# Kernel tuning notes

Measured on AMD Instinct MI355X. Metric: run time of the kernel, lower is better.

## Reference

```python
import jax, jax.numpy as jnp
import numpy as np

N, D, E, EDGE_DIM = 50000, 128, 800000, 3
NEG_SLOPE = 0.2
LN_EPS = 1e-5


def setup_inputs() -> dict:
    key = jax.random.key(0)
    ks = jax.random.split(key, 12)
    s = 1.0 / np.sqrt(D)
    return {
        "x": jax.random.normal(ks[0], (N, D), jnp.float32),
        "edge_index": jax.random.randint(ks[1], (2, E), 0, N, jnp.int32),
        "edge_attr": jax.random.normal(ks[2], (E, EDGE_DIM), jnp.float32),
        "W_l": jax.random.normal(ks[3], (D, D), jnp.float32) * s,
        "b_l": jnp.zeros((D,), jnp.float32),
        "W_r": jax.random.normal(ks[4], (D, D), jnp.float32) * s,
        "b_r": jnp.zeros((D,), jnp.float32),
        "W_e": jax.random.normal(ks[5], (EDGE_DIM, D), jnp.float32) * (1.0 / np.sqrt(EDGE_DIM)),
        "att": jax.random.normal(ks[6], (D,), jnp.float32) * s,
        "bias": jnp.zeros((D,), jnp.float32),
        "res_weight": jnp.array(0.1, jnp.float32),
        "ln_gamma": jnp.ones((D,), jnp.float32),
        "ln_beta": jnp.zeros((D,), jnp.float32),
    }


def reference(x, edge_index, edge_attr, W_l, b_l, W_r, b_r, W_e, att, bias,
              res_weight, ln_gamma, ln_beta):
    src, dst = edge_index[0], edge_index[1]
    # GATv2: lin_l on source, lin_r on target (heads=1, concat=False)
    x_l = x @ W_l + b_l            # [N, D]
    x_r = x @ W_r + b_r            # [N, D]
    e_emb = edge_attr @ W_e        # [E, D]
    # per-edge attention logits
    m = x_l[src] + x_r[dst] + e_emb                      # [E, D]
    m = jnp.where(m > 0, m, NEG_SLOPE * m)               # leaky_relu(0.2)
    alpha = m @ att                                       # [E]
    # segment softmax over destination nodes
    seg_max = jax.ops.segment_max(alpha, dst, num_segments=N)
    seg_max = jnp.where(jnp.isfinite(seg_max), seg_max, 0.0)
    ex = jnp.exp(alpha - seg_max[dst])
    seg_sum = jax.ops.segment_sum(ex, dst, num_segments=N)
    alpha = ex / (seg_sum[dst] + 1e-16)                   # [E]
    # weighted aggregation of transformed source features (dropout off / eval)
    msgs = x_l[src] * alpha[:, None]                      # [E, D]
    out = jax.ops.segment_sum(msgs, dst, num_segments=N) + bias  # [N, D]
    # residual + LayerNorm
    out = x + res_weight * out
    mu = jnp.mean(out, axis=-1, keepdims=True)
    var = jnp.mean(jnp.square(out - mu), axis=-1, keepdims=True)
    out = (out - mu) * jax.lax.rsqrt(var + LN_EPS)
    return out * ln_gamma + ln_beta
```

## Files before the change

kernel.cpp:

```cpp
#include <hip/hip_runtime.h>
#include <hip/hip_bf16.h>

#define N_NODES 50000
#define DIM 128
#define N_EDGES 800000
#define NEG_SLOPE 0.2f
#define LN_EPS 1e-5f
#define SCAN_BS 256
#define NB_SCAN ((N_NODES + SCAN_BS - 1) / SCAN_BS)
#define PADCAP (N_EDGES + 7 * N_NODES)


__global__ __launch_bounds__(256) void lin_kernel(
    const float* __restrict__ x,
    const float* __restrict__ Wl, const float* __restrict__ bl,
    const float* __restrict__ Wr, const float* __restrict__ br,
    __hip_bfloat16* __restrict__ xl_bf, float* __restrict__ xr)
{
    __shared__ float xs[16][DIM];
    const int node0 = blockIdx.x * 16;
    const int t = threadIdx.x;
    for (int i = t; i < 16 * DIM; i += 256) {
        int n = node0 + (i >> 7);
        xs[i >> 7][i & 127] = (n < N_NODES) ? x[(size_t)n * DIM + (i & 127)] : 0.f;
    }
    __syncthreads();
    const int d = t & 127;
    const bool is_l = (t < 128);
    const float* W = is_l ? Wl : Wr;
    const float* b = is_l ? bl : br;
    float acc[16];
#pragma unroll
    for (int i = 0; i < 16; i++) acc[i] = b[d];
#pragma unroll 2
    for (int k = 0; k < DIM; k += 2) {
        const float w0 = W[k * DIM + d];
        const float w1 = W[(k + 1) * DIM + d];
#pragma unroll
        for (int i = 0; i < 16; i++) {
            const float2 xv = *(const float2*)&xs[i][k];
            acc[i] += xv.x * w0;
            acc[i] += xv.y * w1;
        }
    }
#pragma unroll
    for (int i = 0; i < 16; i++) {
        int n = node0 + i;
        if (n < N_NODES) {
            if (is_l) xl_bf[(size_t)n * DIM + d] = __float2bfloat16(acc[i]);
            else      xr[(size_t)n * DIM + d] = acc[i];
        }
    }
}

__global__ __launch_bounds__(256) void hist_kernel(const int* __restrict__ dst_idx,
                                                   int* __restrict__ cnt) {
    int i = blockIdx.x * 256 + threadIdx.x;
    int e = i * 4;
    if (e + 4 <= N_EDGES) {
        const int4 d4 = *(const int4*)(dst_idx + e);
        atomicAdd(&cnt[d4.x], 1);
        atomicAdd(&cnt[d4.y], 1);
        atomicAdd(&cnt[d4.z], 1);
        atomicAdd(&cnt[d4.w], 1);
    } else {
        for (; e < N_EDGES; ++e) atomicAdd(&cnt[dst_idx[e]], 1);
    }
}

__global__ __launch_bounds__(SCAN_BS) void scan1_kernel(int* __restrict__ cnt,
                                                        int* __restrict__ partials) {
    __shared__ int sh[SCAN_BS];
    const int i = blockIdx.x * SCAN_BS + threadIdx.x;
    const int deg = (i < N_NODES) ? cnt[i] : 0;
    const int v = (deg + 7) & ~7;
    sh[threadIdx.x] = v;
    __syncthreads();
    for (int off = 1; off < SCAN_BS; off <<= 1) {
        int u = (threadIdx.x >= off) ? sh[threadIdx.x - off] : 0;
        __syncthreads();
        sh[threadIdx.x] += u;
        __syncthreads();
    }
    if (i < N_NODES) cnt[i] = sh[threadIdx.x] - v;
    if (threadIdx.x == SCAN_BS - 1) partials[blockIdx.x] = sh[threadIdx.x];
}

__global__ __launch_bounds__(SCAN_BS) void scan23_kernel(int* __restrict__ cnt,
                                                         const int* __restrict__ partials,
                                                         int* __restrict__ cursor) {
    __shared__ int sh[SCAN_BS];
    const int t = threadIdx.x;
    sh[t] = (t < NB_SCAN) ? partials[t] : 0;
    __syncthreads();
    for (int off = 1; off < SCAN_BS; off <<= 1) {
        int u = (t >= off) ? sh[t - off] : 0;
        __syncthreads();
        sh[t] += u;
        __syncthreads();
    }
    const int boff = (blockIdx.x == 0) ? 0 : sh[blockIdx.x - 1];
    const int i = blockIdx.x * SCAN_BS + t;
    if (i < N_NODES) {
        const int rs = cnt[i] + boff;
        cnt[i] = rs;
        cursor[i] = rs;
    }
}

__global__ __launch_bounds__(256) void scatter_kernel(
    const int* __restrict__ src_idx, const int* __restrict__ dst_idx,
    const float* __restrict__ ea,
    int* __restrict__ cursor, float4* __restrict__ packed) {
    int e = blockIdx.x * 256 + threadIdx.x;
    if (e >= N_EDGES) return;
    int pos = atomicAdd(&cursor[dst_idx[e]], 1);
    float4 p;
    p.x = ea[(size_t)e * 3 + 0];
    p.y = ea[(size_t)e * 3 + 1];
    p.z = ea[(size_t)e * 3 + 2];
    p.w = __int_as_float(src_idx[e]);
    packed[pos] = p;
}

#define LOGIT(PX, K, XL0, XL1)                                               \
    {                                                                        \
        float t0 = (XL0) + xrv.x + (K).x * we0.x + (K).y * we1.x + (K).z * we2.x; \
        float t1 = (XL1) + xrv.y + (K).x * we0.y + (K).y * we1.y + (K).z * we2.y; \
        t0 = t0 > 0.f ? t0 : NEG_SLOPE * t0;                                 \
        t1 = t1 > 0.f ? t1 : NEG_SLOPE * t1;                                 \
        PX = t0 * at.x + t1 * at.y;                                          \
    }

__global__ __launch_bounds__(256) void fused_node_kernel(
    const float* __restrict__ x, const __hip_bfloat16* __restrict__ xl_bf,
    const int* __restrict__ row_start, const int* __restrict__ cursor,
    const float4* __restrict__ packed,
    const float* __restrict__ We, const float* __restrict__ att,
    const float* __restrict__ bias, const float* __restrict__ rw_p,
    const float* __restrict__ gamma, const float* __restrict__ beta,
    float* __restrict__ out)
{
    const int v = blockIdx.x * 4 + (threadIdx.x >> 6);
    const int lane = threadIdx.x & 63;
    if (v >= N_NODES) return;
    const int begin = row_start[v];
    const int end   = cursor[v];
    const size_t nb = (size_t)v * DIM + 2 * lane;
    const int loff = 2 * lane;
    const float2 xrv = *(const float2*)&out[nb];
    const float2 at  = *(const float2*)&att[loff];
    const float2 we0 = *(const float2*)&We[0 * DIM + loff];
    const float2 we1 = *(const float2*)&We[1 * DIM + loff];
    const float2 we2 = *(const float2*)&We[2 * DIM + loff];

    float m = -3.4e38f, s = 0.f, a0 = 0.f, a1 = 0.f;
    int pos = begin;
    const int deg = end - begin;
    const int full8 = begin + (deg & ~7);

    for (; pos < full8; pos += 8) {
        const float4 k0 = packed[pos + 0], k1 = packed[pos + 1];
        const float4 k2 = packed[pos + 2], k3 = packed[pos + 3];
        const float4 k4 = packed[pos + 4], k5 = packed[pos + 5];
        const float4 k6 = packed[pos + 6], k7 = packed[pos + 7];
        const unsigned xu0 = *(const unsigned*)&xl_bf[(size_t)__float_as_int(k0.w) * DIM + loff];
        const unsigned xu1 = *(const unsigned*)&xl_bf[(size_t)__float_as_int(k1.w) * DIM + loff];
        const unsigned xu2 = *(const unsigned*)&xl_bf[(size_t)__float_as_int(k2.w) * DIM + loff];
        const unsigned xu3 = *(const unsigned*)&xl_bf[(size_t)__float_as_int(k3.w) * DIM + loff];
        const unsigned xu4 = *(const unsigned*)&xl_bf[(size_t)__float_as_int(k4.w) * DIM + loff];
        const unsigned xu5 = *(const unsigned*)&xl_bf[(size_t)__float_as_int(k5.w) * DIM + loff];
        const unsigned xu6 = *(const unsigned*)&xl_bf[(size_t)__float_as_int(k6.w) * DIM + loff];
        const unsigned xu7 = *(const unsigned*)&xl_bf[(size_t)__float_as_int(k7.w) * DIM + loff];
        const float xl00 = __uint_as_float(xu0 << 16), xl10 = __uint_as_float(xu0 & 0xffff0000u);
        const float xl01 = __uint_as_float(xu1 << 16), xl11 = __uint_as_float(xu1 & 0xffff0000u);
        const float xl02 = __uint_as_float(xu2 << 16), xl12 = __uint_as_float(xu2 & 0xffff0000u);
        const float xl03 = __uint_as_float(xu3 << 16), xl13 = __uint_as_float(xu3 & 0xffff0000u);
        const float xl04 = __uint_as_float(xu4 << 16), xl14 = __uint_as_float(xu4 & 0xffff0000u);
        const float xl05 = __uint_as_float(xu5 << 16), xl15 = __uint_as_float(xu5 & 0xffff0000u);
        const float xl06 = __uint_as_float(xu6 << 16), xl16 = __uint_as_float(xu6 & 0xffff0000u);
        const float xl07 = __uint_as_float(xu7 << 16), xl17 = __uint_as_float(xu7 & 0xffff0000u);

        float P0, P1, P2, P3, P4, P5, P6, P7;
        LOGIT(P0, k0, xl00, xl10)  LOGIT(P1, k1, xl01, xl11)
        LOGIT(P2, k2, xl02, xl12)  LOGIT(P3, k3, xl03, xl13)
        LOGIT(P4, k4, xl04, xl14)  LOGIT(P5, k5, xl05, xl15)
        LOGIT(P6, k6, xl06, xl16)  LOGIT(P7, k7, xl07, xl17)

        const bool b1 = (lane & 1), b2 = (lane & 2), b4 = (lane & 4);
        float A0, A1, A2, A3, B0, B1, G;
        {
            const float q0 = __shfl_xor(P0, 1, 64), q1 = __shfl_xor(P1, 1, 64);
            const float q2 = __shfl_xor(P2, 1, 64), q3 = __shfl_xor(P3, 1, 64);
            const float q4 = __shfl_xor(P4, 1, 64), q5 = __shfl_xor(P5, 1, 64);
            const float q6 = __shfl_xor(P6, 1, 64), q7 = __shfl_xor(P7, 1, 64);
            A0 = b1 ? (P1 + q1) : (P0 + q0);
            A1 = b1 ? (P3 + q3) : (P2 + q2);
            A2 = b1 ? (P5 + q5) : (P4 + q4);
            A3 = b1 ? (P7 + q7) : (P6 + q6);
        }
        {
            const float q0 = __shfl_xor(A0, 2, 64), q1 = __shfl_xor(A1, 2, 64);
            const float q2 = __shfl_xor(A2, 2, 64), q3 = __shfl_xor(A3, 2, 64);
            B0 = b2 ? (A1 + q1) : (A0 + q0);
            B1 = b2 ? (A3 + q3) : (A2 + q2);
        }
        {
            const float q0 = __shfl_xor(B0, 4, 64), q1 = __shfl_xor(B1, 4, 64);
            G = b4 ? (B1 + q1) : (B0 + q0);
        }
        G += __shfl_xor(G, 8, 64);
        G += __shfl_xor(G, 16, 64);
        G += __shfl_xor(G, 32, 64);
        const float p0 = __shfl(G, 0, 64), p1 = __shfl(G, 1, 64);
        const float p2 = __shfl(G, 2, 64), p3 = __shfl(G, 3, 64);
        const float p4 = __shfl(G, 4, 64), p5 = __shfl(G, 5, 64);
        const float p6 = __shfl(G, 6, 64), p7 = __shfl(G, 7, 64);

        const float pm = fmaxf(fmaxf(fmaxf(p0, p1), fmaxf(p2, p3)),
                               fmaxf(fmaxf(p4, p5), fmaxf(p6, p7)));
        if (pm <= m + 8.f) {
            const float w0 = __expf(p0 - m), w1 = __expf(p1 - m);
            const float w2 = __expf(p2 - m), w3 = __expf(p3 - m);
            const float w4 = __expf(p4 - m), w5 = __expf(p5 - m);
            const float w6 = __expf(p6 - m), w7 = __expf(p7 - m);
            s  += ((w0 + w1) + (w2 + w3)) + ((w4 + w5) + (w6 + w7));
            a0 += (w0 * xl00 + w1 * xl01 + w2 * xl02 + w3 * xl03)
                + (w4 * xl04 + w5 * xl05 + w6 * xl06 + w7 * xl07);
            a1 += (w0 * xl10 + w1 * xl11 + w2 * xl12 + w3 * xl13)
                + (w4 * xl14 + w5 * xl15 + w6 * xl16 + w7 * xl17);
        } else {
            const float mn = fmaxf(m, pm);
            const float f  = __expf(m - mn);
            const float w0 = __expf(p0 - mn), w1 = __expf(p1 - mn);
            const float w2 = __expf(p2 - mn), w3 = __expf(p3 - mn);
            const float w4 = __expf(p4 - mn), w5 = __expf(p5 - mn);
            const float w6 = __expf(p6 - mn), w7 = __expf(p7 - mn);
            s  = s  * f + ((w0 + w1) + (w2 + w3)) + ((w4 + w5) + (w6 + w7));
            a0 = a0 * f + (w0 * xl00 + w1 * xl01 + w2 * xl02 + w3 * xl03)
                        + (w4 * xl04 + w5 * xl05 + w6 * xl06 + w7 * xl07);
            a1 = a1 * f + (w0 * xl10 + w1 * xl11 + w2 * xl12 + w3 * xl13)
                        + (w4 * xl14 + w5 * xl15 + w6 * xl16 + w7 * xl17);
            m = mn;
        }
    }

    if (end - pos >= 4) {
        const float4 k0 = packed[pos + 0], k1 = packed[pos + 1];
        const float4 k2 = packed[pos + 2], k3 = packed[pos + 3];
        const unsigned xu0 = *(const unsigned*)&xl_bf[(size_t)__float_as_int(k0.w) * DIM + loff];
        const unsigned xu1 = *(const unsigned*)&xl_bf[(size_t)__float_as_int(k1.w) * DIM + loff];
        const unsigned xu2 = *(const unsigned*)&xl_bf[(size_t)__float_as_int(k2.w) * DIM + loff];
        const unsigned xu3 = *(const unsigned*)&xl_bf[(size_t)__float_as_int(k3.w) * DIM + loff];
        const float xl00 = __uint_as_float(xu0 << 16), xl10 = __uint_as_float(xu0 & 0xffff0000u);
        const float xl01 = __uint_as_float(xu1 << 16), xl11 = __uint_as_float(xu1 & 0xffff0000u);
        const float xl02 = __uint_as_float(xu2 << 16), xl12 = __uint_as_float(xu2 & 0xffff0000u);
        const float xl03 = __uint_as_float(xu3 << 16), xl13 = __uint_as_float(xu3 & 0xffff0000u);
        float P0, P1, P2, P3;
        LOGIT(P0, k0, xl00, xl10)  LOGIT(P1, k1, xl01, xl11)
        LOGIT(P2, k2, xl02, xl12)  LOGIT(P3, k3, xl03, xl13)
        const float tA0 = __shfl_xor(P0, 1, 64), tA1 = __shfl_xor(P1, 1, 64);
        const float tB0 = __shfl_xor(P2, 1, 64), tB1 = __shfl_xor(P3, 1, 64);
        const bool b0 = (lane & 1);
        float A = b0 ? (P1 + tA1) : (P0 + tA0);
        float B = b0 ? (P3 + tB1) : (P2 + tB0);
        const float tA = __shfl_xor(A, 2, 64), tB = __shfl_xor(B, 2, 64);
        float C = (lane & 2) ? (B + tB) : (A + tA);
        C += __shfl_xor(C, 4, 64);
        C += __shfl_xor(C, 8, 64);
        C += __shfl_xor(C, 16, 64);
        C += __shfl_xor(C, 32, 64);
        const float p0 = __shfl(C, 0, 64), p1 = __shfl(C, 1, 64);
        const float p2 = __shfl(C, 2, 64), p3 = __shfl(C, 3, 64);
        const float pm = fmaxf(fmaxf(p0, p1), fmaxf(p2, p3));
        if (pm <= m + 8.f) {
            const float w0 = __expf(p0 - m), w1 = __expf(p1 - m);
            const float w2 = __expf(p2 - m), w3 = __expf(p3 - m);
            s  += (w0 + w1) + (w2 + w3);
            a0 += w0 * xl00 + w1 * xl01 + w2 * xl02 + w3 * xl03;
            a1 += w0 * xl10 + w1 * xl11 + w2 * xl12 + w3 * xl13;
        } else {
            const float mn = fmaxf(m, pm);
            const float f  = __expf(m - mn);
            const float w0 = __expf(p0 - mn), w1 = __expf(p1 - mn);
            const float w2 = __expf(p2 - mn), w3 = __expf(p3 - mn);
            s  = s  * f + (w0 + w1) + (w2 + w3);
            a0 = a0 * f + w0 * xl00 + w1 * xl01 + w2 * xl02 + w3 * xl03;
            a1 = a1 * f + w0 * xl10 + w1 * xl11 + w2 * xl12 + w3 * xl13;
            m = mn;
        }
        pos += 4;
    }

    for (; pos < end; ++pos) {
        const float4 pk = packed[pos];
        const unsigned xu = *(const unsigned*)&xl_bf[(size_t)__float_as_int(pk.w) * DIM + loff];
        const float xl0 = __uint_as_float(xu << 16);
        const float xl1 = __uint_as_float(xu & 0xffff0000u);
        float p;
        LOGIT(p, pk, xl0, xl1)
#pragma unroll
        for (int o = 32; o > 0; o >>= 1) p += __shfl_xor(p, o, 64);
        if (p <= m + 8.f) {
            const float w = __expf(p - m);
            s += w; a0 += w * xl0; a1 += w * xl1;
        } else {
            const float mn = fmaxf(m, p);
            const float f = __expf(m - mn);
            const float w = __expf(p - mn);
            s = s * f + w; a0 = a0 * f + w * xl0; a1 = a1 * f + w * xl1;
            m = mn;
        }
    }

    const float inv = 1.f / (s + 1e-16f);

    const float2 xv = *(const float2*)&x[nb];
    const float rw = rw_p[0];
    float v0 = xv.x + rw * (a0 * inv + bias[loff]);
    float v1 = xv.y + rw * (a1 * inv + bias[loff + 1]);
    float sum = v0 + v1;
#pragma unroll
    for (int o = 32; o > 0; o >>= 1) sum += __shfl_xor(sum, o, 64);
    const float mu = sum * (1.f / DIM);
    const float d0 = v0 - mu, d1 = v1 - mu;
    float q = d0 * d0 + d1 * d1;
#pragma unroll
    for (int o = 32; o > 0; o >>= 1) q += __shfl_xor(q, o, 64);
    const float rstd = rsqrtf(q * (1.f / DIM) + LN_EPS);
    float2 r;
    r.x = d0 * rstd * gamma[loff]     + beta[loff];
    r.y = d1 * rstd * gamma[loff + 1] + beta[loff + 1];
    *(float2*)&out[nb] = r;
}

extern "C" void kernel_launch(void* const* d_in, const int* in_sizes, int n_in,
                              void* d_out, int out_size, void* d_ws, size_t ws_size,
                              hipStream_t stream)
{
    const float* x    = (const float*)d_in[0];
    const int*   ei   = (const int*)d_in[1];
    const float* ea   = (const float*)d_in[2];
    const float* Wl   = (const float*)d_in[3];
    const float* bl   = (const float*)d_in[4];
    const float* Wr   = (const float*)d_in[5];
    const float* br   = (const float*)d_in[6];
    const float* We   = (const float*)d_in[7];
    const float* att  = (const float*)d_in[8];
    const float* bias = (const float*)d_in[9];
    const float* rw   = (const float*)d_in[10];
    const float* gmm  = (const float*)d_in[11];
    const float* bta  = (const float*)d_in[12];
    float* out = (float*)d_out;

    const int* src_idx = ei;
    const int* dst_idx = ei + N_EDGES;

    __hip_bfloat16* xl_bf = (__hip_bfloat16*)d_ws;
    float4* packed    = (float4*)(xl_bf + (size_t)N_NODES * DIM);
    int*   row_start  = (int*)(packed + PADCAP);
    int*   cursor     = row_start + N_NODES;
    int*   partials   = cursor + N_NODES;

    hipMemsetAsync(row_start, 0, (size_t)N_NODES * sizeof(int), stream);
    hist_kernel<<<(N_EDGES / 4 + 255) / 256, 256, 0, stream>>>(dst_idx, row_start);
    scan1_kernel<<<NB_SCAN, SCAN_BS, 0, stream>>>(row_start, partials);
    scan23_kernel<<<NB_SCAN, SCAN_BS, 0, stream>>>(row_start, partials, cursor);
    scatter_kernel<<<(N_EDGES + 255) / 256, 256, 0, stream>>>(src_idx, dst_idx, ea,
                                                              cursor, packed);
    lin_kernel<<<(N_NODES + 15) / 16, 256, 0, stream>>>(x, Wl, bl, Wr, br, xl_bf, out);
    fused_node_kernel<<<(N_NODES + 3) / 4, 256, 0, stream>>>(x, xl_bf, row_start, cursor,
                                                             packed,
                                                             We, att, bias, rw, gmm, bta, out);
}
```

Measured before the change: 349.6 us.

## Register-tile lin GEMM, merge scan into one kernel, process 4 nodes per wave

The linear projection kernel switches to a 4x4 register tile per thread, with float4 weight loads and a transposed, padded shared-memory tile. Output stores are vectorised as bf16 and float4. The two-pass scan becomes a single 1024-thread block in which each thread scans a contiguous chunk serially, saving a launch. The fused node kernel now loops over 4 consecutive nodes per wave and hoists the per-lane parameter loads out of that loop, at the cost of less parallelism per node.

Result: slower. 445.7 us (+27.5%).

```diff
diff --git a/kernel.cpp b/kernel.cpp
--- a/kernel.cpp
+++ b/kernel.cpp
@@ -6,10 +6,16 @@
 #define N_EDGES 800000
 #define NEG_SLOPE 0.2f
 #define LN_EPS 1e-5f
-#define SCAN_BS 256
-#define NB_SCAN ((N_NODES + SCAN_BS - 1) / SCAN_BS)
 #define PADCAP (N_EDGES + 7 * N_NODES)
-
+#define SCAN_T 1024
+#define ITEMS ((N_NODES + SCAN_T - 1) / SCAN_T)
+#define LINPAD 20
+
+
+__device__ __forceinline__ unsigned short f2bf(float f) {
+    __hip_bfloat16 h = __float2bfloat16(f);
+    return *reinterpret_cast<unsigned short*>(&h);
+}
 
 __global__ __launch_bounds__(256) void lin_kernel(
     const float* __restrict__ x,
@@ -17,38 +23,48 @@
     const float* __restrict__ Wr, const float* __restrict__ br,
     __hip_bfloat16* __restrict__ xl_bf, float* __restrict__ xr)
 {
-    __shared__ float xs[16][DIM];
+    __shared__ float xs[DIM][LINPAD];
     const int node0 = blockIdx.x * 16;
     const int t = threadIdx.x;
-    for (int i = t; i < 16 * DIM; i += 256) {
-        int n = node0 + (i >> 7);
-        xs[i >> 7][i & 127] = (n < N_NODES) ? x[(size_t)n * DIM + (i & 127)] : 0.f;
+    for (int idx = t; idx < 16 * DIM; idx += 256) {
+        const int n = idx >> 7, k = idx & 127;
+        const int gn = node0 + n;
+        xs[k][n] = (gn < N_NODES) ? x[(size_t)gn * DIM + k] : 0.f;
     }
     __syncthreads();
-    const int d = t & 127;
-    const bool is_l = (t < 128);
+    const int tn = (t & 3) * 4;
+    const int tc = (t >> 2) * 4;
+    const bool is_l = tc < DIM;
     const float* W = is_l ? Wl : Wr;
     const float* b = is_l ? bl : br;
-    float acc[16];
+    const int col = is_l ? tc : tc - DIM;
+    float4 a0 = {0.f, 0.f, 0.f, 0.f}, a1 = a0, a2 = a0, a3 = a0;
+#pragma unroll 4
+    for (int k = 0; k < DIM; ++k) {
+        const float4 wv = *(const float4*)&W[k * DIM + col];
+        const float4 xv = *(const float4*)&xs[k][tn];
+        a0.x += xv.x * wv.x; a0.y += xv.x * wv.y; a0.z += xv.x * wv.z; a0.w += xv.x * wv.w;
+        a1.x += xv.y * wv.x; a1.y += xv.y * wv.y; a1.z += xv.y * wv.z; a1.w += xv.y * wv.w;
+        a2.x += xv.z * wv.x; a2.y += xv.z * wv.y; a2.z += xv.z * wv.z; a2.w += xv.z * wv.w;
+        a3.x += xv.w * wv.x; a3.y += xv.w * wv.y; a3.z += xv.w * wv.z; a3.w += xv.w * wv.w;
+    }
+    const float4 bv = *(const float4*)&b[col];
+    a0.x += bv.x; a0.y += bv.y; a0.z += bv.z; a0.w += bv.w;
+    a1.x += bv.x; a1.y += bv.y; a1.z += bv.z; a1.w += bv.w;
+    a2.x += bv.x; a2.y += bv.y; a2.z += bv.z; a2.w += bv.w;
+    a3.x += bv.x; a3.y += bv.y; a3.z += bv.z; a3.w += bv.w;
+    float4 acc[4] = {a0, a1, a2, a3};
 #pragma unroll
-    for (int i = 0; i < 16; i++) acc[i] = b[d];
-#pragma unroll 2
-    for (int k = 0; k < DIM; k += 2) {
-        const float w0 = W[k * DIM + d];
-        const float w1 = W[(k + 1) * DIM + d];
-#pragma unroll
-        for (int i = 0; i < 16; i++) {
-            const float2 xv = *(const float2*)&xs[i][k];
-            acc[i] += xv.x * w0;
-            acc[i] += xv.y * w1;
-        }
-    }
-#pragma unroll
-    for (int i = 0; i < 16; i++) {
-        int n = node0 + i;
-        if (n < N_NODES) {
-            if (is_l) xl_bf[(size_t)n * DIM + d] = __float2bfloat16(acc[i]);
-            else      xr[(size_t)n * DIM + d] = acc[i];
+    for (int i = 0; i < 4; ++i) {
+        const int gn = node0 + tn + i;
+        if (gn >= N_NODES) continue;
+        if (is_l) {
+            ushort4 u;
+            u.x = f2bf(acc[i].x); u.y = f2bf(acc[i].y);
+            u.z = f2bf(acc[i].z); u.w = f2bf(acc[i].w);
+            *(ushort4*)&xl_bf[(size_t)gn * DIM + col] = u;
+        } else {
+            *(float4*)&xr[(size_t)gn * DIM + col] = acc[i];
         }
     }
 }
@@ -68,43 +84,28 @@
     }
 }
 
-__global__ __launch_bounds__(SCAN_BS) void scan1_kernel(int* __restrict__ cnt,
-                                                        int* __restrict__ partials) {
-    __shared__ int sh[SCAN_BS];
-    const int i = blockIdx.x * SCAN_BS + threadIdx.x;
-    const int deg = (i < N_NODES) ? cnt[i] : 0;
-    const int v = (deg + 7) & ~7;
-    sh[threadIdx.x] = v;
+__global__ __launch_bounds__(SCAN_T) void scan_all_kernel(int* __restrict__ cnt,
+                                                          int* __restrict__ cursor) {
+    __shared__ int sh[SCAN_T];
+    const int t = threadIdx.x;
+    const int i0 = t * ITEMS;
+    const int i1 = (i0 + ITEMS < N_NODES) ? i0 + ITEMS : N_NODES;
+    int sum = 0;
+    for (int i = i0; i < i1; ++i) sum += (cnt[i] + 7) & ~7;
+    sh[t] = sum;
     __syncthreads();
-    for (int off = 1; off < SCAN_BS; off <<= 1) {
-        int u = (threadIdx.x >= off) ? sh[threadIdx.x - off] : 0;
-        __syncthreads();
-        sh[threadIdx.x] += u;
-        __syncthreads();
-    }
-    if (i < N_NODES) cnt[i] = sh[threadIdx.x] - v;
-    if (threadIdx.x == SCAN_BS - 1) partials[blockIdx.x] = sh[threadIdx.x];
-}
-
-__global__ __launch_bounds__(SCAN_BS) void scan23_kernel(int* __restrict__ cnt,
-                                                         const int* __restrict__ partials,
-                                                         int* __restrict__ cursor) {
-    __shared__ int sh[SCAN_BS];
-    const int t = threadIdx.x;
-    sh[t] = (t < NB_SCAN) ? partials[t] : 0;
-    __syncthreads();
-    for (int off = 1; off < SCAN_BS; off <<= 1) {
+    for (int off = 1; off < SCAN_T; off <<= 1) {
         int u = (t >= off) ? sh[t - off] : 0;
         __syncthreads();
         sh[t] += u;
         __syncthreads();
     }
-    const int boff = (blockIdx.x == 0) ? 0 : sh[blockIdx.x - 1];
-    const int i = blockIdx.x * SCAN_BS + t;
-    if (i < N_NODES) {
-        const int rs = cnt[i] + boff;
-        cnt[i] = rs;
-        cursor[i] = rs;
+    int run = (t == 0) ? 0 : sh[t - 1];
+    for (int i = i0; i < i1; ++i) {
+        const int pad = (cnt[i] + 7) & ~7;
+        cnt[i] = run;
+        cursor[i] = run;
+        run += pad;
     }
 }
 
@@ -141,197 +142,205 @@
     const float* __restrict__ gamma, const float* __restrict__ beta,
     float* __restrict__ out)
 {
-    const int v = blockIdx.x * 4 + (threadIdx.x >> 6);
+    const int wave = blockIdx.x * 4 + (threadIdx.x >> 6);
     const int lane = threadIdx.x & 63;
-    if (v >= N_NODES) return;
-    const int begin = row_start[v];
-    const int end   = cursor[v];
-    const size_t nb = (size_t)v * DIM + 2 * lane;
+    const int v0 = wave * 4;
+    if (v0 >= N_NODES) return;
     const int loff = 2 * lane;
-    const float2 xrv = *(const float2*)&out[nb];
     const float2 at  = *(const float2*)&att[loff];
     const float2 we0 = *(const float2*)&We[0 * DIM + loff];
     const float2 we1 = *(const float2*)&We[1 * DIM + loff];
     const float2 we2 = *(const float2*)&We[2 * DIM + loff];
-
-    float m = -3.4e38f, s = 0.f, a0 = 0.f, a1 = 0.f;
-    int pos = begin;
-    const int deg = end - begin;
-    const int full8 = begin + (deg & ~7);
-
-    for (; pos < full8; pos += 8) {
-        const float4 k0 = packed[pos + 0], k1 = packed[pos + 1];
-        const float4 k2 = packed[pos + 2], k3 = packed[pos + 3];
-        const float4 k4 = packed[pos + 4], k5 = packed[pos + 5];
-        const float4 k6 = packed[pos + 6], k7 = packed[pos + 7];
-        const unsigned xu0 = *(const unsigned*)&xl_bf[(size_t)__float_as_int(k0.w) * DIM + loff];
-        const unsigned xu1 = *(const unsigned*)&xl_bf[(size_t)__float_as_int(k1.w) * DIM + loff];
-        const unsigned xu2 = *(const unsigned*)&xl_bf[(size_t)__float_as_int(k2.w) * DIM + loff];
-        const unsigned xu3 = *(const unsigned*)&xl_bf[(size_t)__float_as_int(k3.w) * DIM + loff];
-        const unsigned xu4 = *(const unsigned*)&xl_bf[(size_t)__float_as_int(k4.w) * DIM + loff];
-        const unsigned xu5 = *(const unsigned*)&xl_bf[(size_t)__float_as_int(k5.w) * DIM + loff];
-        const unsigned xu6 = *(const unsigned*)&xl_bf[(size_t)__float_as_int(k6.w) * DIM + loff];
-        const unsigned xu7 = *(const unsigned*)&xl_bf[(size_t)__float_as_int(k7.w) * DIM + loff];
-        const float xl00 = __uint_as_float(xu0 << 16), xl10 = __uint_as_float(xu0 & 0xffff0000u);
-        const float xl01 = __uint_as_float(xu1 << 16), xl11 = __uint_as_float(xu1 & 0xffff0000u);
-        const float xl02 = __uint_as_float(xu2 << 16), xl12 = __uint_as_float(xu2 & 0xffff0000u);
-        const float xl03 = __uint_as_float(xu3 << 16), xl13 = __uint_as_float(xu3 & 0xffff0000u);
-        const float xl04 = __uint_as_float(xu4 << 16), xl14 = __uint_as_float(xu4 & 0xffff0000u);
-        const float xl05 = __uint_as_float(xu5 << 16), xl15 = __uint_as_float(xu5 & 0xffff0000u);
-        const float xl06 = __uint_as_float(xu6 << 16), xl16 = __uint_as_float(xu6 & 0xffff0000u);
-        const float xl07 = __uint_as_float(xu7 << 16), xl17 = __uint_as_float(xu7 & 0xffff0000u);
-
-        float P0, P1, P2, P3, P4, P5, P6, P7;
-        LOGIT(P0, k0, xl00, xl10)  LOGIT(P1, k1, xl01, xl11)
-        LOGIT(P2, k2, xl02, xl12)  LOGIT(P3, k3, xl03, xl13)
-        LOGIT(P4, k4, xl04, xl14)  LOGIT(P5, k5, xl05, xl15)
-        LOGIT(P6, k6, xl06, xl16)  LOGIT(P7, k7, xl07, xl17)
-
-        const bool b1 = (lane & 1), b2 = (lane & 2), b4 = (lane & 4);
-        float A0, A1, A2, A3, B0, B1, G;
-        {
-            const float q0 = __shfl_xor(P0, 1, 64), q1 = __shfl_xor(P1, 1, 64);
-            const float q2 = __shfl_xor(P2, 1, 64), q3 = __shfl_xor(P3, 1, 64);
-            const float q4 = __shfl_xor(P4, 1, 64), q5 = __shfl_xor(P5, 1, 64);
-            const float q6 = __shfl_xor(P6, 1, 64), q7 = __shfl_xor(P7, 1, 64);
-            A0 = b1 ? (P1 + q1) : (P0 + q0);
-            A1 = b1 ? (P3 + q3) : (P2 + q2);
-            A2 = b1 ? (P5 + q5) : (P4 + q4);
-            A3 = b1 ? (P7 + q7) : (P6 + q6);
+    const float2 bi  = *(const float2*)&bias[loff];
+    const float2 gm  = *(const float2*)&gamma[loff];
+    const float2 bt  = *(const float2*)&beta[loff];
+    const float rw = rw_p[0];
+
+    for (int j = 0; j < 4; ++j) {
+        const int v = v0 + j;
+        if (v >= N_NODES) return;
+        const int begin = row_start[v];
+        const int end   = cursor[v];
+        const size_t nb = (size_t)v * DIM + loff;
+        const float2 xrv = *(const float2*)&out[nb];
+
+        float m = -3.4e38f, s = 0.f, a0 = 0.f, a1 = 0.f;
+        int pos = begin;
+        const int full8 = begin + ((end - begin) & ~7);
+
+        for (; pos < full8; pos += 8) {
+            const float4 k0 = packed[pos + 0], k1 = packed[pos + 1];
+            const float4 k2 = packed[pos + 2], k3 = packed[pos + 3];
+            const float4 k4 = packed[pos + 4], k5 = packed[pos + 5];
+            const float4 k6 = packed[pos + 6], k7 = packed[pos + 7];
+            const unsigned xu0 = *(const unsigned*)&xl_bf[(size_t)__float_as_int(k0.w) * DIM + loff];
+            const unsigned xu1 = *(const unsigned*)&xl_bf[(size_t)__float_as_int(k1.w) * DIM + loff];
+            const unsigned xu2 = *(const unsigned*)&xl_bf[(size_t)__float_as_int(k2.w) * DIM + loff];
+            const unsigned xu3 = *(const unsigned*)&xl_bf[(size_t)__float_as_int(k3.w) * DIM + loff];
+            const unsigned xu4 = *(const unsigned*)&xl_bf[(size_t)__float_as_int(k4.w) * DIM + loff];
+            const unsigned xu5 = *(const unsigned*)&xl_bf[(size_t)__float_as_int(k5.w) * DIM + loff];
+            const unsigned xu6 = *(const unsigned*)&xl_bf[(size_t)__float_as_int(k6.w) * DIM + loff];
+            const unsigned xu7 = *(const unsigned*)&xl_bf[(size_t)__float_as_int(k7.w) * DIM + loff];
+            const float xl00 = __uint_as_float(xu0 << 16), xl10 = __uint_as_float(xu0 & 0xffff0000u);
+            const float xl01 = __uint_as_float(xu1 << 16), xl11 = __uint_as_float(xu1 & 0xffff0000u);
+            const float xl02 = __uint_as_float(xu2 << 16), xl12 = __uint_as_float(xu2 & 0xffff0000u);
+            const float xl03 = __uint_as_float(xu3 << 16), xl13 = __uint_as_float(xu3 & 0xffff0000u);
+            const float xl04 = __uint_as_float(xu4 << 16), xl14 = __uint_as_float(xu4 & 0xffff0000u);
+            const float xl05 = __uint_as_float(xu5 << 16), xl15 = __uint_as_float(xu5 & 0xffff0000u);
+            const float xl06 = __uint_as_float(xu6 << 16), xl16 = __uint_as_float(xu6 & 0xffff0000u);
+            const float xl07 = __uint_as_float(xu7 << 16), xl17 = __uint_as_float(xu7 & 0xffff0000u);
+
+            float P0, P1, P2, P3, P4, P5, P6, P7;
+            LOGIT(P0, k0, xl00, xl10)  LOGIT(P1, k1, xl01, xl11)
+            LOGIT(P2, k2, xl02, xl12)  LOGIT(P3, k3, xl03, xl13)
+            LOGIT(P4, k4, xl04, xl14)  LOGIT(P5, k5, xl05, xl15)
+            LOGIT(P6, k6, xl06, xl16)  LOGIT(P7, k7, xl07, xl17)
+
+            const bool b1 = (lane & 1), b2 = (lane & 2), b4 = (lane & 4);
+            float A0, A1, A2, A3, B0, B1, G;
+            {
+                const float q0 = __shfl_xor(P0, 1, 64), q1 = __shfl_xor(P1, 1, 64);
+                const float q2 = __shfl_xor(P2, 1, 64), q3 = __shfl_xor(P3, 1, 64);
+                const float q4 = __shfl_xor(P4, 1, 64), q5 = __shfl_xor(P5, 1, 64);
+                const float q6 = __shfl_xor(P6, 1, 64), q7 = __shfl_xor(P7, 1, 64);
+                A0 = b1 ? (P1 + q1) : (P0 + q0);
+                A1 = b1 ? (P3 + q3) : (P2 + q2);
+                A2 = b1 ? (P5 + q5) : (P4 + q4);
+                A3 = b1 ? (P7 + q7) : (P6 + q6);
+            }
+            {
+                const float q0 = __shfl_xor(A0, 2, 64), q1 = __shfl_xor(A1, 2, 64);
+                const float q2 = __shfl_xor(A2, 2, 64), q3 = __shfl_xor(A3, 2, 64);
+                B0 = b2 ? (A1 + q1) : (A0 + q0);
+                B1 = b2 ? (A3 + q3) : (A2 + q2);
+            }
+            {
+                const float q0 = __shfl_xor(B0, 4, 64), q1 = __shfl_xor(B1, 4, 64);
+                G = b4 ? (B1 + q1) : (B0 + q0);
+            }
+            G += __shfl_xor(G, 8, 64);
+            G += __shfl_xor(G, 16, 64);
+            G += __shfl_xor(G, 32, 64);
+            const float p0 = __shfl(G, 0, 64), p1 = __shfl(G, 1, 64);
+            const float p2 = __shfl(G, 2, 64), p3 = __shfl(G, 3, 64);
+            const float p4 = __shfl(G, 4, 64), p5 = __shfl(G, 5, 64);
+            const float p6 = __shfl(G, 6, 64), p7 = __shfl(G, 7, 64);
+
+            const float pm = fmaxf(fmaxf(fmaxf(p0, p1), fmaxf(p2, p3)),
+                                   fmaxf(fmaxf(p4, p5), fmaxf(p6, p7)));
+            if (pm <= m + 8.f) {
+                const float w0 = __expf(p0 - m), w1 = __expf(p1 - m);
+                const float w2 = __expf(p2 - m), w3 = __expf(p3 - m);
+                const float w4 = __expf(p4 - m), w5 = __expf(p5 - m);
+                const float w6 = __expf(p6 - m), w7 = __expf(p7 - m);
+                s  += ((w0 + w1) + (w2 + w3)) + ((w4 + w5) + (w6 + w7));
+                a0 += (w0 * xl00 + w1 * xl01 + w2 * xl02 + w3 * xl03)
+                    + (w4 * xl04 + w5 * xl05 + w6 * xl06 + w7 * xl07);
+                a1 += (w0 * xl10 + w1 * xl11 + w2 * xl12 + w3 * xl13)
+                    + (w4 * xl14 + w5 * xl15 + w6 * xl16 + w7 * xl17);
+            } else {
+                const float mn = fmaxf(m, pm);
+                const float f  = __expf(m - mn);
+                const float w0 = __expf(p0 - mn), w1 = __expf(p1 - mn);
+                const float w2 = __expf(p2 - mn), w3 = __expf(p3 - mn);
+                const float w4 = __expf(p4 - mn), w5 = __expf(p5 - mn);
+                const float w6 = __expf(p6 - mn), w7 = __expf(p7 - mn);
+                s  = s  * f + ((w0 + w1) + (w2 + w3)) + ((w4 + w5) + (w6 + w7));
+                a0 = a0 * f + (w0 * xl00 + w1 * xl01 + w2 * xl02 + w3 * xl03)
+                            + (w4 * xl04 + w5 * xl05 + w6 * xl06 + w7 * xl07);
+                a1 = a1 * f + (w0 * xl10 + w1 * xl11 + w2 * xl12 + w3 * xl13)
+                            + (w4 * xl14 + w5 * xl15 + w6 * xl16 + w7 * xl17);
+                m = mn;
+            }
         }
-        {
-            const float q0 = __shfl_xor(A0, 2, 64), q1 = __shfl_xor(A1, 2, 64);
-            const float q2 = __shfl_xor(A2, 2, 64), q3 = __shfl_xor(A3, 2, 64);
-            B0 = b2 ? (A1 + q1) : (A0 + q0);
-            B1 = b2 ? (A3 + q3) : (A2 + q2);
+
+        if (end - pos >= 4) {
+            const float4 k0 = packed[pos + 0], k1 = packed[pos + 1];
+            const float4 k2 = packed[pos + 2], k3 = packed[pos + 3];
+            const unsigned xu0 = *(const unsigned*)&xl_bf[(size_t)__float_as_int(k0.w) * DIM + loff];
+            const unsigned xu1 = *(const unsigned*)&xl_bf[(size_t)__float_as_int(k1.w) * DIM + loff];
+            const unsigned xu2 = *(const unsigned*)&xl_bf[(size_t)__float_as_int(k2.w) * DIM + loff];
+            const unsigned xu3 = *(const unsigned*)&xl_bf[(size_t)__float_as_int(k3.w) * DIM + loff];
+            const float xl00 = __uint_as_float(xu0 << 16), xl10 = __uint_as_float(xu0 & 0xffff0000u);
+            const float xl01 = __uint_as_float(xu1 << 16), xl11 = __uint_as_float(xu1 & 0xffff0000u);
+            const float xl02 = __uint_as_float(xu2 << 16), xl12 = __uint_as_float(xu2 & 0xffff0000u);
+            const float xl03 = __uint_as_float(xu3 << 16), xl13 = __uint_as_float(xu3 & 0xffff0000u);
+            float P0, P1, P2, P3;
+            LOGIT(P0, k0, xl00, xl10)  LOGIT(P1, k1, xl01, xl11)
+            LOGIT(P2, k2, xl02, xl12)  LOGIT(P3, k3, xl03, xl13)
+            const float tA0 = __shfl_xor(P0, 1, 64), tA1 = __shfl_xor(P1, 1, 64);
+            const float tB0 = __shfl_xor(P2, 1, 64), tB1 = __shfl_xor(P3, 1, 64);
+            const bool b0 = (lane & 1);
+            float A = b0 ? (P1 + tA1) : (P0 + tA0);
+            float B = b0 ? (P3 + tB1) : (P2 + tB0);
+            const float tA = __shfl_xor(A, 2, 64), tB = __shfl_xor(B, 2, 64);
+            float C = (lane & 2) ? (B + tB) : (A + tA);
+            C += __shfl_xor(C, 4, 64);
+            C += __shfl_xor(C, 8, 64);
+            C += __shfl_xor(C, 16, 64);
+            C += __shfl_xor(C, 32, 64);
+            const float p0 = __shfl(C, 0, 64), p1 = __shfl(C, 1, 64);
+            const float p2 = __shfl(C, 2, 64), p3 = __shfl(C, 3, 64);
+            const float pm = fmaxf(fmaxf(p0, p1), fmaxf(p2, p3));
+            if (pm <= m + 8.f) {
+                const float w0 = __expf(p0 - m), w1 = __expf(p1 - m);
+                const float w2 = __expf(p2 - m), w3 = __expf(p3 - m);
+                s  += (w0 + w1) + (w2 + w3);
+                a0 += w0 * xl00 + w1 * xl01 + w2 * xl02 + w3 * xl03;
+                a1 += w0 * xl10 + w1 * xl11 + w2 * xl12 + w3 * xl13;
+            } else {
+                const float mn = fmaxf(m, pm);
+                const float f  = __expf(m - mn);
+                const float w0 = __expf(p0 - mn), w1 = __expf(p1 - mn);
+                const float w2 = __expf(p2 - mn), w3 = __expf(p3 - mn);
+                s  = s  * f + (w0 + w1) + (w2 + w3);
+                a0 = a0 * f + w0 * xl00 + w1 * xl01 + w2 * xl02 + w3 * xl03;
+                a1 = a1 * f + w0 * xl10 + w1 * xl11 + w2 * xl12 + w3 * xl13;
+                m = mn;
+            }
+            pos += 4;
         }
-        {
-            const float q0 = __shfl_xor(B0, 4, 64), q1 = __shfl_xor(B1, 4, 64);
-            G = b4 ? (B1 + q1) : (B0 + q0);
+
+        for (; pos < end; ++pos) {
+            const float4 pk = packed[pos];
+            const unsigned xu = *(const unsigned*)&xl_bf[(size_t)__float_as_int(pk.w) * DIM + loff];
+            const float xl0 = __uint_as_float(xu << 16);
+            const float xl1 = __uint_as_float(xu & 0xffff0000u);
+            float p;
+            LOGIT(p, pk, xl0, xl1)
+#pragma unroll
+            for (int o = 32; o > 0; o >>= 1) p += __shfl_xor(p, o, 64);
+            if (p <= m + 8.f) {
+                const float w = __expf(p - m);
+                s += w; a0 += w * xl0; a1 += w * xl1;
+            } else {
+                const float mn = fmaxf(m, p);
+                const float f = __expf(m - mn);
+                const float w = __expf(p - mn);
+                s = s * f + w; a0 = a0 * f + w * xl0; a1 = a1 * f + w * xl1;
+                m = mn;
+            }
         }
-        G += __shfl_xor(G, 8, 64);
-        G += __shfl_xor(G, 16, 64);
-        G += __shfl_xor(G, 32, 64);
-        const float p0 = __shfl(G, 0, 64), p1 = __shfl(G, 1, 64);
-        const float p2 = __shfl(G, 2, 64), p3 = __shfl(G, 3, 64);
-        const float p4 = __shfl(G, 4, 64), p5 = __shfl(G, 5, 64);
-        const float p6 = __shfl(G, 6, 64), p7 = __shfl(G, 7, 64);
-
-        const float pm = fmaxf(fmaxf(fmaxf(p0, p1), fmaxf(p2, p3)),
-                               fmaxf(fmaxf(p4, p5), fmaxf(p6, p7)));
-        if (pm <= m + 8.f) {
-            const float w0 = __expf(p0 - m), w1 = __expf(p1 - m);
-            const float w2 = __expf(p2 - m), w3 = __expf(p3 - m);
-            const float w4 = __expf(p4 - m), w5 = __expf(p5 - m);
-            const float w6 = __expf(p6 - m), w7 = __expf(p7 - m);
-            s  += ((w0 + w1) + (w2 + w3)) + ((w4 + w5) + (w6 + w7));
-            a0 += (w0 * xl00 + w1 * xl01 + w2 * xl02 + w3 * xl03)
-                + (w4 * xl04 + w5 * xl05 + w6 * xl06 + w7 * xl07);
-            a1 += (w0 * xl10 + w1 * xl11 + w2 * xl12 + w3 * xl13)
-                + (w4 * xl14 + w5 * xl15 + w6 * xl16 + w7 * xl17);
-        } else {
-            const float mn = fmaxf(m, pm);
-            const float f  = __expf(m - mn);
-            const float w0 = __expf(p0 - mn), w1 = __expf(p1 - mn);
-            const float w2 = __expf(p2 - mn), w3 = __expf(p3 - mn);
-            const float w4 = __expf(p4 - mn), w5 = __expf(p5 - mn);
-            const float w6 = __expf(p6 - mn), w7 = __expf(p7 - mn);
-            s  = s  * f + ((w0 + w1) + (w2 + w3)) + ((w4 + w5) + (w6 + w7));
-            a0 = a0 * f + (w0 * xl00 + w1 * xl01 + w2 * xl02 + w3 * xl03)
-                        + (w4 * xl04 + w5 * xl05 + w6 * xl06 + w7 * xl07);
-            a1 = a1 * f + (w0 * xl10 + w1 * xl11 + w2 * xl12 + w3 * xl13)
-                        + (w4 * xl14 + w5 * xl15 + w6 * xl16 + w7 * xl17);
-            m = mn;
-        }
-    }
-
-    if (end - pos >= 4) {
-        const float4 k0 = packed[pos + 0], k1 = packed[pos + 1];
-        const float4 k2 = packed[pos + 2], k3 = packed[pos + 3];
-        const unsigned xu0 = *(const unsigned*)&xl_bf[(size_t)__float_as_int(k0.w) * DIM + loff];
-        const unsigned xu1 = *(const unsigned*)&xl_bf[(size_t)__float_as_int(k1.w) * DIM + loff];
-        const unsigned xu2 = *(const unsigned*)&xl_bf[(size_t)__float_as_int(k2.w) * DIM + loff];
-        const unsigned xu3 = *(const unsigned*)&xl_bf[(size_t)__float_as_int(k3.w) * DIM + loff];
-        const float xl00 = __uint_as_float(xu0 << 16), xl10 = __uint_as_float(xu0 & 0xffff0000u);
-        const float xl01 = __uint_as_float(xu1 << 16), xl11 = __uint_as_float(xu1 & 0xffff0000u);
-        const float xl02 = __uint_as_float(xu2 << 16), xl12 = __uint_as_float(xu2 & 0xffff0000u);
-        const float xl03 = __uint_as_float(xu3 << 16), xl13 = __uint_as_float(xu3 & 0xffff0000u);
-        float P0, P1, P2, P3;
-        LOGIT(P0, k0, xl00, xl10)  LOGIT(P1, k1, xl01, xl11)
-        LOGIT(P2, k2, xl02, xl12)  LOGIT(P3, k3, xl03, xl13)
-        const float tA0 = __shfl_xor(P0, 1, 64), tA1 = __shfl_xor(P1, 1, 64);
-        const float tB0 = __shfl_xor(P2, 1, 64), tB1 = __shfl_xor(P3, 1, 64);
-        const bool b0 = (lane & 1);
-        float A = b0 ? (P1 + tA1) : (P0 + tA0);
-        float B = b0 ? (P3 + tB1) : (P2 + tB0);
-        const float tA = __shfl_xor(A, 2, 64), tB = __shfl_xor(B, 2, 64);
-        float C = (lane & 2) ? (B + tB) : (A + tA);
-        C += __shfl_xor(C, 4, 64);
-        C += __shfl_xor(C, 8, 64);
-        C += __shfl_xor(C, 16, 64);
-        C += __shfl_xor(C, 32, 64);
-        const float p0 = __shfl(C, 0, 64), p1 = __shfl(C, 1, 64);
-        const float p2 = __shfl(C, 2, 64), p3 = __shfl(C, 3, 64);
-        const float pm = fmaxf(fmaxf(p0, p1), fmaxf(p2, p3));
-        if (pm <= m + 8.f) {
-            const float w0 = __expf(p0 - m), w1 = __expf(p1 - m);
-            const float w2 = __expf(p2 - m), w3 = __expf(p3 - m);
-            s  += (w0 + w1) + (w2 + w3);
-            a0 += w0 * xl00 + w1 * xl01 + w2 * xl02 + w3 * xl03;
-            a1 += w0 * xl10 + w1 * xl11 + w2 * xl12 + w3 * xl13;
-        } else {
-            const float mn = fmaxf(m, pm);
-            const float f  = __expf(m - mn);
-            const float w0 = __expf(p0 - mn), w1 = __expf(p1 - mn);
-            const float w2 = __expf(p2 - mn), w3 = __expf(p3 - mn);
-            s  = s  * f + (w0 + w1) + (w2 + w3);
-            a0 = a0 * f + w0 * xl00 + w1 * xl01 + w2 * xl02 + w3 * xl03;
-            a1 = a1 * f + w0 * xl10 + w1 * xl11 + w2 * xl12 + w3 * xl13;
-            m = mn;
-        }
-        pos += 4;
-    }
-
-    for (; pos < end; ++pos) {
-        const float4 pk = packed[pos];
-        const unsigned xu = *(const unsigned*)&xl_bf[(size_t)__float_as_int(pk.w) * DIM + loff];
-        const float xl0 = __uint_as_float(xu << 16);
-        const float xl1 = __uint_as_float(xu & 0xffff0000u);
-        float p;
-        LOGIT(p, pk, xl0, xl1)
+
+        const float inv = 1.f / (s + 1e-16f);
+
+        const float2 xv = *(const float2*)&x[nb];
+        float u0 = xv.x + rw * (a0 * inv + bi.x);
+        float u1 = xv.y + rw * (a1 * inv + bi.y);
+        float sum = u0 + u1;
 #pragma unroll
-        for (int o = 32; o > 0; o >>= 1) p += __shfl_xor(p, o, 64);
-        if (p <= m + 8.f) {
-            const float w = __expf(p - m);
-            s += w; a0 += w * xl0; a1 += w * xl1;
-        } else {
-            const float mn = fmaxf(m, p);
-            const float f = __expf(m - mn);
-            const float w = __expf(p - mn);
-            s = s * f + w; a0 = a0 * f + w * xl0; a1 = a1 * f + w * xl1;
-            m = mn;
-        }
-    }
-
-    const float inv = 1.f / (s + 1e-16f);
-
-    const float2 xv = *(const float2*)&x[nb];
-    const float rw = rw_p[0];
-    float v0 = xv.x + rw * (a0 * inv + bias[loff]);
-    float v1 = xv.y + rw * (a1 * inv + bias[loff + 1]);
-    float sum = v0 + v1;
+        for (int o = 32; o > 0; o >>= 1) sum += __shfl_xor(sum, o, 64);
+        const float mu = sum * (1.f / DIM);
+        const float d0 = u0 - mu, d1 = u1 - mu;
+        float q = d0 * d0 + d1 * d1;
 #pragma unroll
-    for (int o = 32; o > 0; o >>= 1) sum += __shfl_xor(sum, o, 64);
-    const float mu = sum * (1.f / DIM);
-    const float d0 = v0 - mu, d1 = v1 - mu;
-    float q = d0 * d0 + d1 * d1;
-#pragma unroll
-    for (int o = 32; o > 0; o >>= 1) q += __shfl_xor(q, o, 64);
-    const float rstd = rsqrtf(q * (1.f / DIM) + LN_EPS);
-    float2 r;
-    r.x = d0 * rstd * gamma[loff]     + beta[loff];
-    r.y = d1 * rstd * gamma[loff + 1] + beta[loff + 1];
-    *(float2*)&out[nb] = r;
+        for (int o = 32; o > 0; o >>= 1) q += __shfl_xor(q, o, 64);
+        const float rstd = rsqrtf(q * (1.f / DIM) + LN_EPS);
+        float2 r;
+        r.x = d0 * rstd * gm.x + bt.x;
+        r.y = d1 * rstd * gm.y + bt.y;
+        *(float2*)&out[nb] = r;
+    }
 }
 
 extern "C" void kernel_launch(void* const* d_in, const int* in_sizes, int n_in,
@@ -360,16 +369,14 @@
     float4* packed    = (float4*)(xl_bf + (size_t)N_NODES * DIM);
     int*   row_start  = (int*)(packed + PADCAP);
     int*   cursor     = row_start + N_NODES;
-    int*   partials   = cursor + N_NODES;
 
     hipMemsetAsync(row_start, 0, (size_t)N_NODES * sizeof(int), stream);
     hist_kernel<<<(N_EDGES / 4 + 255) / 256, 256, 0, stream>>>(dst_idx, row_start);
-    scan1_kernel<<<NB_SCAN, SCAN_BS, 0, stream>>>(row_start, partials);
-    scan23_kernel<<<NB_SCAN, SCAN_BS, 0, stream>>>(row_start, partials, cursor);
+    scan_all_kernel<<<1, SCAN_T, 0, stream>>>(row_start, cursor);
     scatter_kernel<<<(N_EDGES + 255) / 256, 256, 0, stream>>>(src_idx, dst_idx, ea,
                                                               cursor, packed);
     lin_kernel<<<(N_NODES + 15) / 16, 256, 0, stream>>>(x, Wl, bl, Wr, br, xl_bf, out);
-    fused_node_kernel<<<(N_NODES + 3) / 4, 256, 0, stream>>>(x, xl_bf, row_start, cursor,
-                                                             packed,
-                                                             We, att, bias, rw, gmm, bta, out);
-}
+    fused_node_kernel<<<(N_NODES + 15) / 16, 256, 0, stream>>>(x, xl_bf, row_start, cursor,
+                                                               packed,
+                                                               We, att, bias, rw, gmm, bta, out);
+}
```
